# Kernel tuning notes

Measured on AMD Instinct MI355X. Metric: run time of the kernel, lower is better.

The kernel has to match this reference:

```python
import jax, jax.numpy as jnp
import numpy as np

B, NQ, NK = 4, 1024, 1536
DQ = DK = DV = 1024
DI = 4096
H = 16
EPS = 1e-5

def _ln(x, g, b):
    mu = jnp.mean(x, axis=-1, keepdims=True)
    var = jnp.mean((x - mu) ** 2, axis=-1, keepdims=True)
    return (x - mu) * jax.lax.rsqrt(var + EPS) * g + b

def setup_inputs() -> dict:
    key = jax.random.key(0)
    ks = jax.random.split(key, 20)
    s = 0.02
    inp = {
        "Q": jax.random.normal(ks[0], (B, NQ, DQ), jnp.float32),
        "K": jax.random.normal(ks[1], (B, NK, DK), jnp.float32),
        "knn_masks": jax.random.normal(ks[2], (B * H, NQ, 1024), jnp.float32),
        "mask_pos": 1024,
        "Wq": jax.random.normal(ks[3], (DQ, DV), jnp.float32) * s,
        "bq": jnp.zeros((DV,), jnp.float32),
        "Wk": jax.random.normal(ks[4], (DK, DV), jnp.float32) * s,
        "bk": jnp.zeros((DV,), jnp.float32),
        "Wv": jax.random.normal(ks[5], (DK, DV), jnp.float32) * s,
        "bv": jnp.zeros((DV,), jnp.float32),
        "Wo0": jax.random.normal(ks[6], (DV, DV), jnp.float32) * s,
        "bo0": jnp.zeros((DV,), jnp.float32),
        "Wo": jax.random.normal(ks[7], (DV, DI), jnp.float32) * s,
        "bo": jnp.zeros((DI,), jnp.float32),
        "Wo2": jax.random.normal(ks[8], (DI, DV), jnp.float32) * s,
        "bo2": jnp.zeros((DV,), jnp.float32),
        "g0": jnp.ones((DV,), jnp.float32),
        "beta0": jnp.zeros((DV,), jnp.float32),
        "g1": jnp.ones((DV,), jnp.float32),
        "beta1": jnp.zeros((DV,), jnp.float32),
    }
    return inp

def reference(Q, K, knn_masks, mask_pos, Wq, bq, Wk, bk, Wv, bv,
              Wo0, bo0, Wo, bo, Wo2, bo2, g0, beta0, g1, beta1):
    dh = DV // H
    q = Q @ Wq + bq                      # [B,NQ,DV]
    k = K @ Wk + bk                      # [B,NK,DV]
    v = K @ Wv + bv
    # torch cat(split(.,dh,2),0) -> head-major [H,B,N,dh]
    qh = q.reshape(B, NQ, H, dh).transpose(2, 0, 1, 3)
    kh = k[:, :mask_pos].reshape(B, mask_pos, H, dh).transpose(2, 0, 1, 3)
    vh = v[:, :mask_pos].reshape(B, mask_pos, H, dh).transpose(2, 0, 1, 3)
    logits = jnp.einsum("hbqd,hbkd->hbqk", qh, kh) / jnp.sqrt(jnp.float32(DV))
    logits = logits + knn_masks.reshape(H, B, NQ, mask_pos)
    attn = jax.nn.softmax(logits, axis=-1)
    o = jnp.einsum("hbqk,hbkd->hbqd", attn, vh)   # [H,B,NQ,dh]
    o = o.transpose(1, 2, 0, 3).reshape(B, NQ, DV)  # concat heads
    o = o @ Wo0 + bo0
    O = q + o
    O = _ln(O, g0, beta0)
    ff = jax.nn.relu(O @ Wo + bo) @ Wo2 + bo2
    O = O + ff
    O = _ln(O, g1, beta1)
    return O
```

## Files before the change

kernel.cpp:

```cpp
#include <hip/hip_runtime.h>
#include <hip/hip_bf16.h>

typedef unsigned short u16;
typedef __attribute__((ext_vector_type(4))) short bf16x4;
typedef __attribute__((ext_vector_type(8))) short bf16x8;
typedef __attribute__((ext_vector_type(4))) float f32x4;

static __device__ __forceinline__ u16 f2b(float f){
  union { float f; unsigned u; } v; v.f = f;
  unsigned r = v.u + 0x7fffu + ((v.u >> 16) & 1u);
  return (u16)(r >> 16);
}
static __device__ __forceinline__ float b2f(u16 h){
  union { unsigned u; float f; } v; v.u = ((unsigned)h) << 16; return v.f;
}
static __device__ __forceinline__ void gld_lds16(const void* g, void* l){
  __builtin_amdgcn_global_load_lds((const __attribute__((address_space(1))) void*)g,
                                   (__attribute__((address_space(3))) void*)l, 16, 0, 0);
}

__global__ __launch_bounds__(256) void prep(const float* __restrict__ Q,
                                            const float* __restrict__ K,
                                            u16* __restrict__ Qb, u16* __restrict__ Kb,
                                            const float* __restrict__ Wq, u16* __restrict__ Wq_t,
                                            const float* __restrict__ Wk, u16* __restrict__ Wk_t,
                                            const float* __restrict__ Wv, u16* __restrict__ Wv_t){
  __shared__ float tile[64][65];
  const int id = blockIdx.x, t = threadIdx.x;
  if (id < 8192){
    const float* src; u16* dst;
    if (id < 4096){
      src = Q + (size_t)id * 1024; dst = Qb + (size_t)id * 1024;
    } else {
      int r = id - 4096;
      size_t ir = (size_t)r + (size_t)(r >> 10) * 512;
      src = K + ir * 1024; dst = Kb + (size_t)r * 1024;
    }
    const float4 v = *(const float4*)(src + t * 4);
    bf16x4 o;
    o[0] = (short)f2b(v.x); o[1] = (short)f2b(v.y);
    o[2] = (short)f2b(v.z); o[3] = (short)f2b(v.w);
    *(bf16x4*)(dst + t * 4) = o;
    return;
  }
  int wid = id - 8192;
  int sel = wid >> 8, local = wid & 255;
  int bx = local & 15, by = local >> 4;
  const float* in  = (sel == 0) ? Wq   : (sel == 1) ? Wk   : Wv;
  u16*         out = (sel == 0) ? Wq_t : (sel == 1) ? Wk_t : Wv_t;
  const int k0 = by * 64, n0 = bx * 64;
  const int tr = t >> 4, tc = t & 15;
#pragma unroll
  for (int i = 0; i < 4; i++){
    int r = tr + i * 16;
    float4 v = *(const float4*)(in + (size_t)(k0 + r) * 1024 + n0 + tc * 4);
    tile[r][tc*4+0] = v.x; tile[r][tc*4+1] = v.y; tile[r][tc*4+2] = v.z; tile[r][tc*4+3] = v.w;
  }
  __syncthreads();
#pragma unroll
  for (int i = 0; i < 4; i++){
    int nr = tr + i * 16;
    bf16x4 pk;
#pragma unroll
    for (int j = 0; j < 4; j++) pk[j] = (short)f2b(tile[tc*4+j][nr]);
    *(bf16x4*)(out + (size_t)(n0 + nr) * 1024 + k0 + tc * 4) = pk;
  }
}

static __device__ __forceinline__ void loop8p(const u16* __restrict__ A,
                                              const u16* __restrict__ Bt,
                                              int lda, int ldb, int kbeg, int NT,
                                              int m0, int n0,
                                              u16 (*sA)[2][8192], u16 (*sB)[2][8192],
                                              f32x4 acc[8][4]){
  const int t = threadIdx.x, w = t >> 6, l = t & 63;
  const int wr = w >> 2, wc = w & 3;
  const int c = l & 15, g = l >> 4;
  const int sr = t >> 3, scb = (t & 7) << 4;

  auto stA = [&](int d, int h, int T){
#pragma unroll
    for (int i = 0; i < 2; i++){
      int row = i * 64 + sr;
      int Lb  = scb ^ ((row & 7) << 4);
      gld_lds16(A + (size_t)(m0 + h * 128 + row) * lda + kbeg + T * 64 + (Lb >> 1),
                (char*)&sA[d][h][0] + i * 8192 + t * 16);
    }
  };
  auto stB = [&](int d, int h, int T){
#pragma unroll
    for (int i = 0; i < 2; i++){
      int row = i * 64 + sr;
      int Lb  = scb ^ ((row & 7) << 4);
      gld_lds16(Bt + (size_t)(n0 + h * 128 + row) * ldb + kbeg + T * 64 + (Lb >> 1),
                (char*)&sB[d][h][0] + i * 8192 + t * 16);
    }
  };

  stB(0, 0, 0); stB(0, 1, 0); stA(0, 0, 0); stA(0, 1, 0);
  stB(1, 0, 1); stB(1, 1, 1);

  bf16x8 bfr[4][2];
  for (int T = 0; T < NT; ++T){
    const int d = T & 1;
    const char* pa = (const char*)&sA[d][wr][0];
    const char* pb = (const char*)&sB[d][wc >> 1][0];
#pragma unroll
    for (int q = 0; q < 4; ++q){
      if (q == 0){
        if (T + 1 < NT) asm volatile("s_waitcnt vmcnt(4)" ::: "memory");
        else            asm volatile("s_waitcnt vmcnt(0)" ::: "memory");
        asm volatile("" ::: "memory");
        __builtin_amdgcn_s_barrier();
        asm volatile("" ::: "memory");
#pragma unroll
        for (int nf = 0; nf < 4; ++nf){
          int lr = (wc & 1) * 64 + nf * 16 + c;
#pragma unroll
          for (int ks = 0; ks < 2; ++ks)
            bfr[nf][ks] = *(const bf16x8*)(pb + lr * 128 + ((ks * 64 + g * 16) ^ ((lr & 7) << 4)));
        }
      }
      bf16x8 af[2][2];
#pragma unroll
      for (int mi = 0; mi < 2; ++mi){
        int lr = (q * 2 + mi) * 16 + c;
#pragma unroll
        for (int ks = 0; ks < 2; ++ks)
          af[mi][ks] = *(const bf16x8*)(pa + lr * 128 + ((ks * 64 + g * 16) ^ ((lr & 7) << 4)));
      }
      if      (q == 0){ if (T + 1 < NT) stA(d ^ 1, 0, T + 1); }
      else if (q == 1){ if (T + 1 < NT) stA(d ^ 1, 1, T + 1); }
      else if (q == 2){ if (T + 2 < NT) stB(d, 0, T + 2); }
      else            { if (T + 2 < NT) stB(d, 1, T + 2); }
      __builtin_amdgcn_s_setprio(1);
#pragma unroll
      for (int mi = 0; mi < 2; ++mi)
#pragma unroll
        for (int nf = 0; nf < 4; ++nf)
#pragma unroll
          for (int ks = 0; ks < 2; ++ks)
            acc[q * 2 + mi][nf] =
              __builtin_amdgcn_mfma_f32_16x16x32_bf16(af[mi][ks], bfr[nf][ks], acc[q * 2 + mi][nf], 0, 0, 0);
      __builtin_amdgcn_s_setprio(0);
      asm volatile("" ::: "memory");
      __builtin_amdgcn_s_barrier();
      asm volatile("" ::: "memory");
    }
  }
}

template<typename F>
static __device__ __forceinline__ void epi_store(char* sl, u16* gbase, int ld,
                                                 int l, F val){
  const int c = l & 15, g = l >> 4;
#pragma unroll
  for (int p = 0; p < 2; ++p){
#pragma unroll
    for (int mi = 0; mi < 4; ++mi){
#pragma unroll
      for (int nf = 0; nf < 4; ++nf){
        int col2 = (nf * 16 + c) * 2;
#pragma unroll
        for (int r = 0; r < 4; ++r){
          int row = mi * 16 + 4 * g + r;
          *(u16*)(sl + row * 128 + (col2 ^ ((row & 7) << 4))) = f2b(val(p * 4 + mi, nf, r));
        }
      }
    }
    asm volatile("s_waitcnt lgkmcnt(0)" ::: "memory");
    __builtin_amdgcn_sched_barrier(0);
#pragma unroll
    for (int j = 0; j < 8; ++j){
      int row = (l >> 3) + j * 8;
      int ch  = (l & 7) * 16;
      bf16x8 v = *(const bf16x8*)(sl + row * 128 + (ch ^ ((row & 7) << 4)));
      *(bf16x8*)(gbase + (size_t)(p * 64 + row) * ld + (l & 7) * 8) = v;
    }
    __builtin_amdgcn_sched_barrier(0);
  }
}

template<int EPI>
__global__ __launch_bounds__(512, 2) void gemm8p(const u16* __restrict__ A,
                                                 const u16* __restrict__ Bt,
                                                 const float* __restrict__ bias,
                                                 void* __restrict__ outp,
                                                 int lda, int ldb, int ldout,
                                                 int ksz, int NT){
  __shared__ u16 sA[2][2][8192];
  __shared__ u16 sB[2][2][8192];
  const int t = threadIdx.x, w = t >> 6, l = t & 63;
  const int wr = w >> 2, wc = w & 3;
  const int c = l & 15;

  int m0, n0, zidx;
  if (EPI == 0){
    int lid = blockIdx.x + (blockIdx.y << 4);
    int xcd = lid & 7, slot = lid >> 3;
    int bx = ((xcd & 1) << 3) + (slot & 7);
    int by = ((xcd >> 1) << 2) + (slot >> 3);
    m0 = by * 256; n0 = bx * 256; zidx = 0;
  } else {
    int lid = blockIdx.x + (blockIdx.y << 2) + (blockIdx.z << 6);
    int xcd = lid & 7, slot = lid >> 3;
    int bx = slot & 3, rest = slot >> 2;
    int by = (xcd << 1) + (rest & 1);
    zidx = rest >> 1;
    m0 = by * 256; n0 = bx * 256;
  }

  f32x4 acc[8][4];
#pragma unroll
  for (int i = 0; i < 8; i++)
#pragma unroll
    for (int j = 0; j < 4; j++) acc[i][j] = (f32x4){0.f, 0.f, 0.f, 0.f};

  loop8p(A, Bt, lda, ldb, zidx * ksz, NT, m0, n0, sA, sB, acc);

  char* slw = (char*)&sA[0][0][0] + w * 8192;
  if (EPI == 0){
    float bv[4];
#pragma unroll
    for (int nf = 0; nf < 4; ++nf) bv[nf] = bias[n0 + wc * 64 + nf * 16 + c];
    u16* gb = (u16*)outp + (size_t)(m0 + wr * 128) * ldout + n0 + wc * 64;
    epi_store(slw, gb, ldout, l,
              [&](int mf, int nf, int r){ return fmaxf(acc[mf][nf][r] + bv[nf], 0.f); });
  } else {
    u16* gb = (u16*)outp + (size_t)zidx * (4096ull * 1024ull)
              + (size_t)(m0 + wr * 128) * 1024 + n0 + wc * 64;
    epi_store(slw, gb, 1024, l,
              [&](int mf, int nf, int r){ return acc[mf][nf][r]; });
  }
}

__global__ __launch_bounds__(512, 2) void gemm8p_qkv(const u16* __restrict__ Qb,
                                                     const u16* __restrict__ Kb,
                                                     const u16* __restrict__ Wq_t,
                                                     const u16* __restrict__ Wk_t,
                                                     const u16* __restrict__ Wv_t,
                                                     const float* __restrict__ bq,
                                                     const float* __restrict__ bk,
                                                     const float* __restrict__ bv,
                                                     u16* __restrict__ qb,
                                                     u16* __restrict__ kbf,
                                                     u16* __restrict__ vtb,
                                                     const float* __restrict__ Wo0, u16* __restrict__ Wo0_t,
                                                     const float* __restrict__ Wo,  u16* __restrict__ Wo_t,
                                                     const float* __restrict__ Wo2, u16* __restrict__ Wo2_t){
  __shared__ u16 sA[2][2][8192];
  __shared__ u16 sB[2][2][8192];
  const int id = blockIdx.x, t = threadIdx.x;

  if (id >= 192){
    const int half = t >> 8, tt = t & 255;
    const int tileid = (id - 192) * 2 + half;
    const float* in; u16* out; int Kd, N, bx, by;
    if (tileid < 256){
      bx = tileid & 15; by = tileid >> 4; Kd = 1024; N = 1024; in = Wo0; out = Wo0_t;
    } else if (tileid < 1280){
      int lo = tileid - 256; bx = lo & 63; by = lo >> 6; Kd = 1024; N = 4096; in = Wo; out = Wo_t;
    } else {
      int lo = tileid - 1280; bx = lo & 15; by = lo >> 4; Kd = 4096; N = 1024; in = Wo2; out = Wo2_t;
    }
    u16* tl = (u16*)&sA[0][0][0] + half * 4160;
    const int k0 = by * 64, n0 = bx * 64;
    const int tr = tt >> 4, tc = tt & 15;
#pragma unroll
    for (int i = 0; i < 4; i++){
      int r = tr + i * 16;
      float4 v = *(const float4*)(in + (size_t)(k0 + r) * N + n0 + tc * 4);
      tl[r * 65 + tc * 4 + 0] = f2b(v.x); tl[r * 65 + tc * 4 + 1] = f2b(v.y);
      tl[r * 65 + tc * 4 + 2] = f2b(v.z); tl[r * 65 + tc * 4 + 3] = f2b(v.w);
    }
    __syncthreads();
#pragma unroll
    for (int i = 0; i < 4; i++){
      int nr = tr + i * 16;
      bf16x4 pk;
#pragma unroll
      for (int j = 0; j < 4; j++) pk[j] = (short)tl[(tc * 4 + j) * 65 + nr];
      *(bf16x4*)(out + (size_t)(n0 + nr) * Kd + k0 + tc * 4) = pk;
    }
    return;
  }

  int lid = id;
  int xcd = lid & 7, slot = lid >> 3;
  int bx = (xcd & 3) * 3 + slot % 3;
  int by = ((xcd >> 2) << 3) + slot / 3;
  const int sel = bx >> 2;
  const u16* A    = sel ? Kb : Qb;
  const u16* Bt   = (sel == 0) ? Wq_t : (sel == 1) ? Wk_t : Wv_t;
  const float* bi = (sel == 0) ? bq   : (sel == 1) ? bk   : bv;
  const int w = t >> 6, l = t & 63;
  const int wr = w >> 2, wc = w & 3;
  const int c = l & 15, g = l >> 4;
  const int m0 = by * 256, n0 = (bx & 3) * 256;

  f32x4 acc[8][4];
#pragma unroll
  for (int i = 0; i < 8; i++)
#pragma unroll
    for (int j = 0; j < 4; j++) acc[i][j] = (f32x4){0.f, 0.f, 0.f, 0.f};

  loop8p(A, Bt, 1024, 1024, 0, 16, m0, n0, sA, sB, acc);

  if (sel == 2){
    u16* sl = (w < 4) ? (&sA[0][0][0] + w * 8192) : (&sB[0][0][0] + (w - 4) * 8192);
#pragma unroll
    for (int nf = 0; nf < 4; ++nf){
      int n = n0 + wc * 64 + nf * 16 + c;
      float bv_ = bi[n];
#pragma unroll
      for (int mf = 0; mf < 8; ++mf){
        bf16x4 pk;
#pragma unroll
        for (int r = 0; r < 4; ++r) pk[r] = (short)f2b(acc[mf][nf][r] + bv_);
        *(bf16x4*)(sl + (nf * 16 + c) * 128 + mf * 16 + 4 * g) = pk;
      }
    }
    asm volatile("s_waitcnt lgkmcnt(0)" ::: "memory");
    __builtin_amdgcn_sched_barrier(0);
    const int mg = m0 + wr * 128;
    const int bb = mg >> 10, kb0 = mg & 1023;
    u16* vbase = vtb + ((size_t)bb << 20) + kb0;
#pragma unroll
    for (int j = 0; j < 16; ++j){
      int nl  = (l >> 4) + j * 4;
      int kl  = (l & 15) * 8;
      bf16x8 v = *(const bf16x8*)(sl + nl * 128 + kl);
      *(bf16x8*)(vbase + (size_t)(n0 + wc * 64 + nl) * 1024 + kl) = v;
    }
  } else {
    char* slw = (char*)&sA[0][0][0] + w * 8192;
    float bv[4];
#pragma unroll
    for (int nf = 0; nf < 4; ++nf) bv[nf] = bi[n0 + wc * 64 + nf * 16 + c];
    u16* out = sel ? kbf : qb;
    u16* gb  = out + (size_t)(m0 + wr * 128) * 1024 + n0 + wc * 64;
    epi_store(slw, gb, 1024, l,
              [&](int mf, int nf, int r){ return acc[mf][nf][r] + bv[nf]; });
  }
}

template<int NP, int F32OUT>
__global__ __launch_bounds__(256) void comb_ln(const u16* __restrict__ pp,
                                               const float* __restrict__ bias,
                                               const u16* __restrict__ res,
                                               const float* __restrict__ gw,
                                               const float* __restrict__ bw,
                                               void* __restrict__ outp){
  const int t = threadIdx.x, w = t >> 6;
  const int row = blockIdx.x * 2 + (t >> 7);
  const int u = t & 127;
  const size_t i8 = (size_t)row * 1024 + u * 8;
  bf16x8 rv = *(const bf16x8*)(res + i8);
  float4 b0 = *(const float4*)(bias + u * 8);
  float4 b1 = *(const float4*)(bias + u * 8 + 4);
  float xs[8] = {b0.x, b0.y, b0.z, b0.w, b1.x, b1.y, b1.z, b1.w};
#pragma unroll
  for (int j = 0; j < 8; j++) xs[j] += b2f((u16)rv[j]);
#pragma unroll
  for (int z = 0; z < NP; z++){
    bf16x8 p = *(const bf16x8*)(pp + (size_t)z * (4096ull * 1024ull) + i8);
#pragma unroll
    for (int j = 0; j < 8; j++) xs[j] += b2f((u16)p[j]);
  }
  float s = 0.f, sq = 0.f;
#pragma unroll
  for (int j = 0; j < 8; j++){ s += xs[j]; sq += xs[j] * xs[j]; }
#pragma unroll
  for (int o = 32; o; o >>= 1){ s += __shfl_xor(s, o); sq += __shfl_xor(sq, o); }
  __shared__ float rs[4], rq[4];
  if ((t & 63) == 0){ rs[w] = s; rq[w] = sq; }
  __syncthreads();
  const int wb = (t >> 7) * 2;
  s  = rs[wb] + rs[wb + 1];
  sq = rq[wb] + rq[wb + 1];
  const float mu   = s * (1.f / 1024.f);
  const float var  = sq * (1.f / 1024.f) - mu * mu;
  const float rstd = rsqrtf(var + 1e-5f);
  float4 g0 = *(const float4*)(gw + u * 8);
  float4 g1 = *(const float4*)(gw + u * 8 + 4);
  float4 w0 = *(const float4*)(bw + u * 8);
  float4 w1 = *(const float4*)(bw + u * 8 + 4);
  float gv[8] = {g0.x, g0.y, g0.z, g0.w, g1.x, g1.y, g1.z, g1.w};
  float wv[8] = {w0.x, w0.y, w0.z, w0.w, w1.x, w1.y, w1.z, w1.w};
  if (F32OUT){
    float4 o0, o1;
    o0.x = (xs[0]-mu)*rstd*gv[0] + wv[0]; o0.y = (xs[1]-mu)*rstd*gv[1] + wv[1];
    o0.z = (xs[2]-mu)*rstd*gv[2] + wv[2]; o0.w = (xs[3]-mu)*rstd*gv[3] + wv[3];
    o1.x = (xs[4]-mu)*rstd*gv[4] + wv[4]; o1.y = (xs[5]-mu)*rstd*gv[5] + wv[5];
    o1.z = (xs[6]-mu)*rstd*gv[6] + wv[6]; o1.w = (xs[7]-mu)*rstd*gv[7] + wv[7];
    *(float4*)((float*)outp + i8)     = o0;
    *(float4*)((float*)outp + i8 + 4) = o1;
  } else {
    bf16x8 o;
#pragma unroll
    for (int j = 0; j < 8; j++) o[j] = (short)f2b((xs[j]-mu)*rstd*gv[j] + wv[j]);
    *(bf16x8*)((u16*)outp + i8) = o;
  }
}

#define ATTN_STEP(IT, CUR, MC) do{                                              \
  if ((IT) < 15) asm volatile("s_waitcnt vmcnt(4)" ::: "memory");               \
  else           asm volatile("s_waitcnt vmcnt(0)" ::: "memory");               \
  __builtin_amdgcn_s_barrier();                                                 \
  asm volatile("" ::: "memory");                                                \
  if ((IT) < 15) stage((CUR) ^ 1, ((IT) + 1) * 64);                             \
  asm volatile("" ::: "memory");                                                \
  const char* kt = (const char*)sK[(CUR)];                                      \
  f32x4 st[4];                                                                  \
  _Pragma("unroll")                                                             \
  for (int nf = 0; nf < 4; nf++){                                               \
    const char* kr = kt + (nf * 16 + c) * 128;                                  \
    bf16x8 ak0 = *(const bf16x8*)(kr + ((g * 16) ^ sw));                        \
    bf16x8 ak1 = *(const bf16x8*)(kr + ((64 + g * 16) ^ sw));                   \
    f32x4 z = (f32x4){0.f, 0.f, 0.f, 0.f};                                      \
    z = __builtin_amdgcn_mfma_f32_16x16x32_bf16(ak0, bq0, z, 0, 0, 0);          \
    z = __builtin_amdgcn_mfma_f32_16x16x32_bf16(ak1, bq1, z, 0, 0, 0);          \
    st[nf] = z;                                                                 \
  }                                                                             \
  float rsum = 0.f;                                                             \
  bf16x4 pb[4];                                                                 \
  _Pragma("unroll")                                                             \
  for (int nf = 0; nf < 4; nf++)                                                \
    _Pragma("unroll")                                                           \
    for (int r = 0; r < 4; r++){                                                \
      float p = __expf(fmaf(st[nf][r], 0.03125f, MC[nf][r]) - 8.f);             \
      rsum += p;                                                                \
      pb[nf][r] = (short)f2b(p);                                                \
    }                                                                           \
  if ((IT) < 14){                                                               \
    _Pragma("unroll")                                                           \
    for (int nf = 0; nf < 4; nf++)                                              \
      MC[nf] = *(const f32x4*)(mbase + ((IT) + 2) * 64 + nf * 16 + g * 4);      \
  }                                                                             \
  rsum += __shfl_xor(rsum, 16); rsum += __shfl_xor(rsum, 32);                   \
  lsum += rsum;                                                                 \
  const char* vtc = (const char*)sV[(CUR)];                                     \
  __builtin_amdgcn_s_setprio(1);                                                \
  _Pragma("unroll")                                                             \
  for (int f = 0; f < 4; f++){                                                  \
    const char* vr = vtc + (f * 16 + c) * 128;                                  \
    _Pragma("unroll")                                                           \
    for (int nf = 0; nf < 4; nf++){                                             \
      bf16x4 av = *(const bf16x4*)(vr + ((nf * 32 + g * 8) ^ sw));              \
      acc[f] = __builtin_amdgcn_mfma_f32_16x16x16bf16_1k(av, pb[nf], acc[f], 0, 0, 0); \
    }                                                                           \
  }                                                                             \
  __builtin_amdgcn_s_setprio(0);                                                \
}while(0)

__global__ __launch_bounds__(512, 4) void attn_k(const u16* __restrict__ qb,
                                                 const u16* __restrict__ kb,
                                                 const u16* __restrict__ vt,
                                                 const float* __restrict__ mask,
                                                 u16* __restrict__ ob){
  __shared__ u16 sK[2][4096];
  __shared__ u16 sV[2][4096];

  const int aid = blockIdx.x, t = threadIdx.x;
  const int w = t >> 6, l = t & 63;
  const int c = l & 15, g = l >> 4;
  const int q0 = (aid & 7) * 128;
  const int h  = (aid >> 3) & 15, b = aid >> 7;
  const int qrow = q0 + w * 16 + c;
  const size_t qoff = ((size_t)(b * 1024 + qrow)) * 1024 + h * 64;
  const bf16x8 bq0 = *(const bf16x8*)(qb + qoff + g * 8);
  const bf16x8 bq1 = *(const bf16x8*)(qb + qoff + 32 + g * 8);
  const u16* kbase = kb + ((size_t)b * 1024) * 1024 + h * 64;
  const u16* vbase = vt + ((size_t)b << 20) + (size_t)(h * 64) * 1024;
  const float* mbase = mask + ((size_t)(h * 4 + b) * 1024 + qrow) * 1024;

  const int srow = t >> 3, slc = t & 7;

  auto stage = [&](int buf, int kv){
    int L = (slc * 16) ^ ((srow & 7) << 4);
    gld_lds16(kbase + (size_t)(kv + srow) * 1024 + (L >> 1), &sK[buf][t * 8]);
    gld_lds16(vbase + (size_t)srow * 1024 + kv + (L >> 1),   &sV[buf][t * 8]);
  };

  float lsum = 0.f;
  f32x4 acc[4];
#pragma unroll
  for (int f = 0; f < 4; f++) acc[f] = (f32x4){0.f, 0.f, 0.f, 0.f};

  stage(0, 0);
  asm volatile("" ::: "memory");
  f32x4 mA[4], mB[4];
#pragma unroll
  for (int nf = 0; nf < 4; nf++) mA[nf] = *(const f32x4*)(mbase + nf * 16 + g * 4);
  asm volatile("" ::: "memory");
#pragma unroll
  for (int nf = 0; nf < 4; nf++) mB[nf] = *(const f32x4*)(mbase + 64 + nf * 16 + g * 4);

  const int sw = (c & 7) << 4;
  for (int ii = 0; ii < 8; ++ii){
    ATTN_STEP(2 * ii,     0, mA);
    ATTN_STEP(2 * ii + 1, 1, mB);
  }

  __syncthreads();
  const float inv = 1.f / lsum;
  u16* sO = &sK[0][0];
#pragma unroll
  for (int f = 0; f < 4; f++){
    bf16x4 pk;
#pragma unroll
    for (int r = 0; r < 4; r++) pk[r] = (short)f2b(acc[f][r] * inv);
    *(bf16x4*)(sO + (w * 16 + c) * 64 + f * 16 + 4 * g) = pk;
  }
  asm volatile("s_waitcnt lgkmcnt(0)" ::: "memory");
  __builtin_amdgcn_sched_barrier(0);
  {
    int rl  = w * 16 + (l >> 2);
    int d0  = (l & 3) * 16;
    bf16x8 v0 = *(const bf16x8*)(sO + rl * 64 + d0);
    bf16x8 v1 = *(const bf16x8*)(sO + rl * 64 + d0 + 8);
    u16* dst = ob + ((size_t)(b * 1024 + q0 + rl)) * 1024 + h * 64 + d0;
    *(bf16x8*)(dst)     = v0;
    *(bf16x8*)(dst + 8) = v1;
  }
}

extern "C" void kernel_launch(void* const* d_in, const int* in_sizes, int n_in,
                              void* d_out, int out_size, void* d_ws, size_t ws_size,
                              hipStream_t stream){
  const float* Q    = (const float*)d_in[0];
  const float* K    = (const float*)d_in[1];
  const float* mask = (const float*)d_in[2];
  const float* Wq   = (const float*)d_in[4];  const float* bq  = (const float*)d_in[5];
  const float* Wk   = (const float*)d_in[6];  const float* bk  = (const float*)d_in[7];
  const float* Wv   = (const float*)d_in[8];  const float* bv  = (const float*)d_in[9];
  const float* Wo0  = (const float*)d_in[10]; const float* bo0 = (const float*)d_in[11];
  const float* Wo   = (const float*)d_in[12]; const float* bo  = (const float*)d_in[13];
  const float* Wo2  = (const float*)d_in[14]; const float* bo2 = (const float*)d_in[15];
  const float* g0   = (const float*)d_in[16]; const float* be0 = (const float*)d_in[17];
  const float* g1   = (const float*)d_in[18]; const float* be1 = (const float*)d_in[19];

  uint8_t* W = (uint8_t*)d_ws;
  const size_t MB = 1024ull * 1024ull;
  u16* Wq_t  = (u16*)(W + 0);
  u16* Wk_t  = (u16*)(W + 2  * MB);
  u16* Wv_t  = (u16*)(W + 4  * MB);
  u16* Wo0_t = (u16*)(W + 6  * MB);
  u16* Wo_t  = (u16*)(W + 8  * MB);
  u16* Wo2_t = (u16*)(W + 16 * MB);
  u16* Qb    = (u16*)(W + 24 * MB);
  u16* Kb    = (u16*)(W + 32 * MB);
  u16* qb    = (u16*)(W + 40 * MB);
  u16* kbf   = (u16*)(W + 48 * MB);
  u16* vtb   = (u16*)(W + 56 * MB);
  u16* ob    = (u16*)(W + 24 * MB);
  u16* x1b   = (u16*)(W + 64 * MB);
  u16* hb    = (u16*)(W + 32 * MB);
  u16* ppb   = (u16*)(W + 72 * MB);

  prep<<<8960, 256, 0, stream>>>(Q, K, Qb, Kb, Wq, Wq_t, Wk, Wk_t, Wv, Wv_t);

  gemm8p_qkv<<<1344, 512, 0, stream>>>(Qb, Kb, Wq_t, Wk_t, Wv_t,
                                       bq, bk, bv, qb, kbf, vtb,
                                       Wo0, Wo0_t, Wo, Wo_t, Wo2, Wo2_t);

  attn_k<<<512, 512, 0, stream>>>(qb, kbf, vtb, mask, ob);

  gemm8p<1><<<dim3(4, 16, 4), 512, 0, stream>>>(ob, Wo0_t, nullptr, ppb, 1024, 1024, 1024, 256, 4);
  comb_ln<4, 0><<<2048, 256, 0, stream>>>(ppb, bo0, qb, g0, be0, x1b);

  gemm8p<0><<<dim3(16, 16), 512, 0, stream>>>(x1b, Wo_t, bo, hb, 1024, 1024, 4096, 0, 16);
  gemm8p<1><<<dim3(4, 16, 4), 512, 0, stream>>>(hb, Wo2_t, nullptr, ppb, 4096, 4096, 1024, 1024, 16);
  comb_ln<4, 1><<<2048, 256, 0, stream>>>(ppb, bo2, x1b, g1, be1, d_out);
}
```

Baseline: 260.4 us.

## Swap MFMA operands for direct epilogue stores, batch prep rows, reorder attention MFMAs

The prep kernel now converts eight rows of Q/K per block instead of one, which reduces the launch grid. The output GEMMs swap the MFMA A/B operands so each lane holds four consecutive columns. This lets the epilogue write bf16x4 directly to global memory and skip the LDS-staged transpose store. The attention kernel loads all K fragments for each k-half before issuing its MFMAs, and reorders the PV loop so independent accumulators interleave. These changes aim to cut LDS round-trips and MFMA dependency stalls, at the cost of narrower 8-byte global stores and more registers held live.

```diff
diff --git a/kernel.cpp b/kernel.cpp
--- a/kernel.cpp
+++ b/kernel.cpp
@@ -27,23 +27,27 @@
                                             const float* __restrict__ Wv, u16* __restrict__ Wv_t){
   __shared__ float tile[64][65];
   const int id = blockIdx.x, t = threadIdx.x;
-  if (id < 8192){
-    const float* src; u16* dst;
-    if (id < 4096){
-      src = Q + (size_t)id * 1024; dst = Qb + (size_t)id * 1024;
-    } else {
-      int r = id - 4096;
-      size_t ir = (size_t)r + (size_t)(r >> 10) * 512;
-      src = K + ir * 1024; dst = Kb + (size_t)r * 1024;
-    }
-    const float4 v = *(const float4*)(src + t * 4);
-    bf16x4 o;
-    o[0] = (short)f2b(v.x); o[1] = (short)f2b(v.y);
-    o[2] = (short)f2b(v.z); o[3] = (short)f2b(v.w);
-    *(bf16x4*)(dst + t * 4) = o;
+  if (id < 1024){
+#pragma unroll
+    for (int i = 0; i < 8; i++){
+      int row = id * 8 + i;
+      const float* src; u16* dst;
+      if (row < 4096){
+        src = Q + (size_t)row * 1024; dst = Qb + (size_t)row * 1024;
+      } else {
+        int r = row - 4096;
+        size_t ir = (size_t)r + (size_t)(r >> 10) * 512;
+        src = K + ir * 1024; dst = Kb + (size_t)r * 1024;
+      }
+      const float4 v = *(const float4*)(src + t * 4);
+      bf16x4 o;
+      o[0] = (short)f2b(v.x); o[1] = (short)f2b(v.y);
+      o[2] = (short)f2b(v.z); o[3] = (short)f2b(v.w);
+      *(bf16x4*)(dst + t * 4) = o;
+    }
     return;
   }
-  int wid = id - 8192;
+  int wid = id - 1024;
   int sel = wid >> 8, local = wid & 255;
   int bx = local & 15, by = local >> 4;
   const float* in  = (sel == 0) ? Wq   : (sel == 1) ? Wk   : Wv;
@@ -67,6 +71,7 @@
   }
 }
 
+template<int SWAP>
 static __device__ __forceinline__ void loop8p(const u16* __restrict__ A,
                                               const u16* __restrict__ Bt,
                                               int lda, int ldb, int kbeg, int NT,
@@ -135,13 +140,14 @@
       else            { if (T + 2 < NT) stB(d, 1, T + 2); }
       __builtin_amdgcn_s_setprio(1);
 #pragma unroll
-      for (int mi = 0; mi < 2; ++mi)
-#pragma unroll
-        for (int nf = 0; nf < 4; ++nf)
-#pragma unroll
-          for (int ks = 0; ks < 2; ++ks)
-            acc[q * 2 + mi][nf] =
-              __builtin_amdgcn_mfma_f32_16x16x32_bf16(af[mi][ks], bfr[nf][ks], acc[q * 2 + mi][nf], 0, 0, 0);
+      for (int ks = 0; ks < 2; ++ks)
+#pragma unroll
+        for (int mi = 0; mi < 2; ++mi)
+#pragma unroll
+          for (int nf = 0; nf < 4; ++nf)
+            acc[q * 2 + mi][nf] = SWAP
+              ? __builtin_amdgcn_mfma_f32_16x16x32_bf16(bfr[nf][ks], af[mi][ks], acc[q * 2 + mi][nf], 0, 0, 0)
+              : __builtin_amdgcn_mfma_f32_16x16x32_bf16(af[mi][ks], bfr[nf][ks], acc[q * 2 + mi][nf], 0, 0, 0);
       __builtin_amdgcn_s_setprio(0);
       asm volatile("" ::: "memory");
       __builtin_amdgcn_s_barrier();
@@ -192,7 +198,7 @@
   __shared__ u16 sB[2][2][8192];
   const int t = threadIdx.x, w = t >> 6, l = t & 63;
   const int wr = w >> 2, wc = w & 3;
-  const int c = l & 15;
+  const int c = l & 15, g = l >> 4;
 
   int m0, n0, zidx;
   if (EPI == 0){
@@ -216,21 +222,37 @@
 #pragma unroll
     for (int j = 0; j < 4; j++) acc[i][j] = (f32x4){0.f, 0.f, 0.f, 0.f};
 
-  loop8p(A, Bt, lda, ldb, zidx * ksz, NT, m0, n0, sA, sB, acc);
-
-  char* slw = (char*)&sA[0][0][0] + w * 8192;
+  loop8p<1>(A, Bt, lda, ldb, zidx * ksz, NT, m0, n0, sA, sB, acc);
+
+  const int mb = m0 + wr * 128 + c;
+  const int nb = n0 + wc * 64 + 4 * g;
   if (EPI == 0){
-    float bv[4];
-#pragma unroll
-    for (int nf = 0; nf < 4; ++nf) bv[nf] = bias[n0 + wc * 64 + nf * 16 + c];
-    u16* gb = (u16*)outp + (size_t)(m0 + wr * 128) * ldout + n0 + wc * 64;
-    epi_store(slw, gb, ldout, l,
-              [&](int mf, int nf, int r){ return fmaxf(acc[mf][nf][r] + bv[nf], 0.f); });
+    float4 bv4[4];
+#pragma unroll
+    for (int nf = 0; nf < 4; ++nf) bv4[nf] = *(const float4*)(bias + nb + nf * 16);
+    u16* ob_ = (u16*)outp;
+#pragma unroll
+    for (int mf = 0; mf < 8; ++mf)
+#pragma unroll
+      for (int nf = 0; nf < 4; ++nf){
+        bf16x4 pk;
+        pk[0] = (short)f2b(fmaxf(acc[mf][nf][0] + bv4[nf].x, 0.f));
+        pk[1] = (short)f2b(fmaxf(acc[mf][nf][1] + bv4[nf].y, 0.f));
+        pk[2] = (short)f2b(fmaxf(acc[mf][nf][2] + bv4[nf].z, 0.f));
+        pk[3] = (short)f2b(fmaxf(acc[mf][nf][3] + bv4[nf].w, 0.f));
+        *(bf16x4*)(ob_ + (size_t)(mb + mf * 16) * ldout + nb + nf * 16) = pk;
+      }
   } else {
-    u16* gb = (u16*)outp + (size_t)zidx * (4096ull * 1024ull)
-              + (size_t)(m0 + wr * 128) * 1024 + n0 + wc * 64;
-    epi_store(slw, gb, 1024, l,
-              [&](int mf, int nf, int r){ return acc[mf][nf][r]; });
+    u16* po = (u16*)outp + (size_t)zidx * (4096ull * 1024ull);
+#pragma unroll
+    for (int mf = 0; mf < 8; ++mf)
+#pragma unroll
+      for (int nf = 0; nf < 4; ++nf){
+        bf16x4 pk;
+#pragma unroll
+        for (int r = 0; r < 4; ++r) pk[r] = (short)f2b(acc[mf][nf][r]);
+        *(bf16x4*)(po + (size_t)(mb + mf * 16) * 1024 + nb + nf * 16) = pk;
+      }
   }
 }
 
@@ -304,7 +326,7 @@
 #pragma unroll
     for (int j = 0; j < 4; j++) acc[i][j] = (f32x4){0.f, 0.f, 0.f, 0.f};
 
-  loop8p(A, Bt, 1024, 1024, 0, 16, m0, n0, sA, sB, acc);
+  loop8p<0>(A, Bt, 1024, 1024, 0, 16, m0, n0, sA, sB, acc);
 
   if (sel == 2){
     u16* sl = (w < 4) ? (&sA[0][0][0] + w * 8192) : (&sB[0][0][0] + (w - 4) * 8192);
@@ -411,17 +433,22 @@
   if ((IT) < 15) stage((CUR) ^ 1, ((IT) + 1) * 64);                             \
   asm volatile("" ::: "memory");                                                \
   const char* kt = (const char*)sK[(CUR)];                                      \
+  bf16x8 ak[4];                                                                 \
   f32x4 st[4];                                                                  \
   _Pragma("unroll")                                                             \
+  for (int nf = 0; nf < 4; nf++)                                                \
+    ak[nf] = *(const bf16x8*)(kt + (nf * 16 + c) * 128 + ((g * 16) ^ sw));      \
+  _Pragma("unroll")                                                             \
   for (int nf = 0; nf < 4; nf++){                                               \
-    const char* kr = kt + (nf * 16 + c) * 128;                                  \
-    bf16x8 ak0 = *(const bf16x8*)(kr + ((g * 16) ^ sw));                        \
-    bf16x8 ak1 = *(const bf16x8*)(kr + ((64 + g * 16) ^ sw));                   \
     f32x4 z = (f32x4){0.f, 0.f, 0.f, 0.f};                                      \
-    z = __builtin_amdgcn_mfma_f32_16x16x32_bf16(ak0, bq0, z, 0, 0, 0);          \
-    z = __builtin_amdgcn_mfma_f32_16x16x32_bf16(ak1, bq1, z, 0, 0, 0);          \
-    st[nf] = z;                                                                 \
+    st[nf] = __builtin_amdgcn_mfma_f32_16x16x32_bf16(ak[nf], bq0, z, 0, 0, 0);  \
   }                                                                             \
+  _Pragma("unroll")                                                             \
+  for (int nf = 0; nf < 4; nf++)                                                \
+    ak[nf] = *(const bf16x8*)(kt + (nf * 16 + c) * 128 + ((64 + g * 16) ^ sw)); \
+  _Pragma("unroll")                                                             \
+  for (int nf = 0; nf < 4; nf++)                                                \
+    st[nf] = __builtin_amdgcn_mfma_f32_16x16x32_bf16(ak[nf], bq1, st[nf], 0, 0, 0); \
   float rsum = 0.f;                                                             \
   bf16x4 pb[4];                                                                 \
   _Pragma("unroll")                                                             \
@@ -442,10 +469,10 @@
   const char* vtc = (const char*)sV[(CUR)];                                     \
   __builtin_amdgcn_s_setprio(1);                                                \
   _Pragma("unroll")                                                             \
-  for (int f = 0; f < 4; f++){                                                  \
-    const char* vr = vtc + (f * 16 + c) * 128;                                  \
+  for (int nf = 0; nf < 4; nf++){                                               \
     _Pragma("unroll")                                                           \
-    for (int nf = 0; nf < 4; nf++){                                             \
+    for (int f = 0; f < 4; f++){                                                \
+      const char* vr = vtc + (f * 16 + c) * 128;                                \
       bf16x4 av = *(const bf16x4*)(vr + ((nf * 32 + g * 8) ^ sw));              \
       acc[f] = __builtin_amdgcn_mfma_f32_16x16x16bf16_1k(av, pb[nf], acc[f], 0, 0, 0); \
     }                                                                           \
@@ -558,7 +585,7 @@
   u16* hb    = (u16*)(W + 32 * MB);
   u16* ppb   = (u16*)(W + 72 * MB);
 
-  prep<<<8960, 256, 0, stream>>>(Q, K, Qb, Kb, Wq, Wq_t, Wk, Wk_t, Wv, Wv_t);
+  prep<<<1792, 256, 0, stream>>>(Q, K, Qb, Kb, Wq, Wq_t, Wk, Wk_t, Wv, Wv_t);
 
   gemm8p_qkv<<<1344, 512, 0, stream>>>(Qb, Kb, Wq_t, Wk_t, Wv_t,
                                        bq, bk, bv, qb, kbf, vtb,
```

After: 262.8 us. About the same (+0.9%).
